# Kernel optimization log

Hardware: AMD Instinct MI355X
Metric: run time of the kernel (lower is better)

The kernel has to match this reference:

```python
import jax, jax.numpy as jnp
import numpy as np

NUM_HEADS = 16
HEAD_DIM = 64
D_MODEL = NUM_HEADS * HEAD_DIM  # 1024
TOP_K_TILES = 8
TILE_SIZE = 16


def setup_inputs() -> dict:
    key = jax.random.key(0)
    kx, kq, kk, kv, ko = jax.random.split(key, 5)
    B, S = 2, 2048
    scale = 1.0 / np.sqrt(D_MODEL)
    return {
        "x": jax.random.normal(kx, (B, S, D_MODEL), dtype=jnp.float32),
        "wq": jax.random.normal(kq, (D_MODEL, NUM_HEADS * HEAD_DIM), dtype=jnp.float32) * scale,
        "wk": jax.random.normal(kk, (D_MODEL, NUM_HEADS * HEAD_DIM), dtype=jnp.float32) * scale,
        "wv": jax.random.normal(kv, (D_MODEL, NUM_HEADS * HEAD_DIM), dtype=jnp.float32) * scale,
        "wo": jax.random.normal(ko, (NUM_HEADS * HEAD_DIM, D_MODEL), dtype=jnp.float32) * scale,
    }


def reference(x, wq, wk, wv, wo):
    B, S, _ = x.shape
    H, D = NUM_HEADS, HEAD_DIM
    q = (x @ wq).reshape(B, S, H, D)
    k = (x @ wk).reshape(B, S, H, D)
    v = (x @ wv).reshape(B, S, H, D)
    logits = jnp.einsum('bqhd,bkhd->bhqk', q, k) / jnp.sqrt(jnp.float32(D))
    causal = jnp.tril(jnp.ones((S, S), dtype=bool))
    logits = jnp.where(causal[None, None, :, :], logits, jnp.float32(-1e10))
    weights = jax.nn.softmax(logits, axis=-1)  # [B,H,S,S]

    # tile pooling + top-k on the last query row (auxiliary output, cached in original)
    last_token_probs = weights[:, :, -1, :]  # [B,H,S]
    pad_len = (TILE_SIZE - S % TILE_SIZE) % TILE_SIZE
    if pad_len > 0:
        last_token_probs = jnp.pad(last_token_probs, ((0, 0), (0, 0), (0, pad_len)))
    num_tiles = last_token_probs.shape[-1] // TILE_SIZE
    tile_scores = last_token_probs.reshape(B, H, num_tiles, TILE_SIZE).max(axis=-1)
    _, top_tile_indices = jax.lax.top_k(tile_scores, TOP_K_TILES)  # side output
    del top_tile_indices  # original stores in a global cache; not returned

    out = jnp.einsum('bhqk,bkhd->bqhd', weights, v).reshape(B, S, H * D)
    return out @ wo
```

## Files before the change

kernel.cpp:

```cpp
#include <hip/hip_runtime.h>
#include <hip/hip_bf16.h>

#define NUM_HEADS 16
#define HEAD_DIM 64
#define DMODEL 1024
#define SEQ 2048
#define BATCH 2
#define MROWS (BATCH*SEQ)

typedef __bf16 bf16;
typedef __bf16 bf16x4 __attribute__((ext_vector_type(4)));
typedef __bf16 bf16x8 __attribute__((ext_vector_type(8)));
typedef float f32x4 __attribute__((ext_vector_type(4)));

#define MFMA16(a, b, c) __builtin_amdgcn_mfma_f32_16x16x32_bf16((a), (b), (c), 0, 0, 0)

#define QSCALE 0.1803368801111444f

__device__ __forceinline__ float fast_exp2(float x) {
    float r;
    asm("v_exp_f32 %0, %1" : "=v"(r) : "v"(x));
    return r;
}

__device__ __forceinline__ void gld16(const void* g, void* l) {
    __builtin_amdgcn_global_load_lds(
        (const __attribute__((address_space(1))) void*)g,
        (__attribute__((address_space(3))) void*)l, 16, 0, 0);
}


__global__ __launch_bounds__(256) void cvt_f32_bf16(const float* __restrict__ in,
                                                    bf16* __restrict__ out, int n4) {
    int i = blockIdx.x * 256 + threadIdx.x;
    if (i >= n4) return;
    float4 v = *(const float4*)(in + (size_t)i * 4);
    bf16x4 o = { (bf16)v.x, (bf16)v.y, (bf16)v.z, (bf16)v.w };
    *(bf16x4*)(out + (size_t)i * 4) = o;
}

__global__ __launch_bounds__(256) void cvt_trans(const float* __restrict__ w0, const float* __restrict__ w1,
                                                 const float* __restrict__ w2, const float* __restrict__ w3,
                                                 bf16* __restrict__ o0, bf16* __restrict__ o1,
                                                 bf16* __restrict__ o2, bf16* __restrict__ o3) {
    const float* w = blockIdx.z == 0 ? w0 : blockIdx.z == 1 ? w1 : blockIdx.z == 2 ? w2 : w3;
    bf16* o = blockIdx.z == 0 ? o0 : blockIdx.z == 1 ? o1 : blockIdx.z == 2 ? o2 : o3;
    __shared__ bf16 tile[64][65];
    int k0 = blockIdx.y * 64, n0 = blockIdx.x * 64;
    int tc = threadIdx.x & 63;
    int tr0 = threadIdx.x >> 6;
#pragma unroll
    for (int i = 0; i < 16; i++) {
        int r = tr0 + i * 4;
        tile[r][tc] = (bf16)w[(size_t)(k0 + r) * DMODEL + n0 + tc];
    }
    __syncthreads();
#pragma unroll
    for (int i = 0; i < 16; i++) {
        int r = tr0 + i * 4;
        o[(size_t)(n0 + r) * DMODEL + k0 + tc] = tile[tc][r];
    }
}


#define BM 128
#define BN 128
#define BK 32

__device__ __forceinline__ void gemm_core(const bf16* __restrict__ A, const bf16* __restrict__ Bt,
                                          int m0, int n0, int Kdim,
                                          bf16* As, bf16* Bs, f32x4 acc[4][4]) {
    int t = threadIdx.x;
    int lane = t & 63;
    int wave = t >> 6;
    int wm = (wave >> 1) * 64;
    int wn = (wave & 1) * 64;
#pragma unroll
    for (int mf = 0; mf < 4; mf++)
#pragma unroll
        for (int nf = 0; nf < 4; nf++) acc[mf][nf] = (f32x4){0.f, 0.f, 0.f, 0.f};

    int arow = lane & 15, kg = lane >> 4;

    for (int k0 = 0; k0 < Kdim; k0 += BK) {
        __syncthreads();
#pragma unroll
        for (int it = 0; it < 2; it++) {
            int chunk = it * 256 + t;
            int rr = chunk >> 2, cc = chunk & 3;
            gld16(A + (size_t)(m0 + rr) * Kdim + k0 + cc * 8, As + chunk * 8);
            gld16(Bt + (size_t)(n0 + rr) * Kdim + k0 + cc * 8, Bs + chunk * 8);
        }
        __syncthreads();
        bf16x8 af[4], bfr[4];
#pragma unroll
        for (int mf = 0; mf < 4; mf++)
            af[mf] = *(const bf16x8*)(As + (wm + mf * 16 + arow) * BK + kg * 8);
#pragma unroll
        for (int nf = 0; nf < 4; nf++)
            bfr[nf] = *(const bf16x8*)(Bs + (wn + nf * 16 + arow) * BK + kg * 8);
#pragma unroll
        for (int mf = 0; mf < 4; mf++)
#pragma unroll
            for (int nf = 0; nf < 4; nf++)
                acc[mf][nf] = MFMA16(af[mf], bfr[nf], acc[mf][nf]);
    }
}

__global__ __launch_bounds__(256) void gemm_qkv(const bf16* __restrict__ xb,
                                                const bf16* __restrict__ wqT, const bf16* __restrict__ wkT,
                                                const bf16* __restrict__ wvT,
                                                bf16* __restrict__ Qh, bf16* __restrict__ Kh,
                                                bf16* __restrict__ Vt) {
    __shared__ __attribute__((aligned(16))) bf16 As[BM * BK];
    __shared__ __attribute__((aligned(16))) bf16 Bs[BN * BK];
    int z = blockIdx.z;
    const bf16* Bt = z == 0 ? wqT : z == 1 ? wkT : wvT;
    int m0 = blockIdx.y * BM, n0 = blockIdx.x * BN;
    f32x4 acc[4][4];
    gemm_core(xb, Bt, m0, n0, DMODEL, As, Bs, acc);

    int lane = threadIdx.x & 63, wave = threadIdx.x >> 6;
    int wm = (wave >> 1) * 64, wn = (wave & 1) * 64;
    int col0 = n0 + wn + (lane & 15);
    int row0 = m0 + wm + (lane >> 4) * 4;
    if (z < 2) {
        bf16* O = z == 0 ? Qh : Kh;
        float scl = z == 0 ? QSCALE : 1.0f;
#pragma unroll
        for (int mf = 0; mf < 4; mf++)
#pragma unroll
            for (int nf = 0; nf < 4; nf++) {
                int n = col0 + nf * 16;
                int mb = row0 + mf * 16;
                int hh = n >> 6, d = n & 63;
#pragma unroll
                for (int i2 = 0; i2 < 4; i2++) {
                    int m = mb + i2;
                    int bb = m >> 11, s = m & 2047;
                    O[(((size_t)bb * NUM_HEADS + hh) * SEQ + s) * HEAD_DIM + d] =
                        (bf16)(acc[mf][nf][i2] * scl);
                }
            }
    } else {
#pragma unroll
        for (int mf = 0; mf < 4; mf++)
#pragma unroll
            for (int nf = 0; nf < 4; nf++) {
                int n = col0 + nf * 16;
                int m = row0 + mf * 16;
                int b = m >> 11, s = m & 2047;
                int h = n >> 6, d = n & 63;
                bf16x4 pack = { (bf16)acc[mf][nf][0], (bf16)acc[mf][nf][1],
                                (bf16)acc[mf][nf][2], (bf16)acc[mf][nf][3] };
                *(bf16x4*)(Vt + ((size_t)(b * NUM_HEADS + h) * HEAD_DIM + d) * SEQ + s) = pack;
            }
    }
}

__global__ __launch_bounds__(256) void gemm_outp(const bf16* __restrict__ at,
                                                 const bf16* __restrict__ woT,
                                                 float* __restrict__ out) {
    __shared__ __attribute__((aligned(16))) bf16 As[BM * BK];
    __shared__ __attribute__((aligned(16))) bf16 Bs[BN * BK];
    int m0 = blockIdx.y * BM, n0 = blockIdx.x * BN;
    f32x4 acc[4][4];
    gemm_core(at, woT, m0, n0, DMODEL, As, Bs, acc);

    int lane = threadIdx.x & 63, wave = threadIdx.x >> 6;
    int wm = (wave >> 1) * 64, wn = (wave & 1) * 64;
    int col0 = n0 + wn + (lane & 15);
    int row0 = m0 + wm + (lane >> 4) * 4;
#pragma unroll
    for (int mf = 0; mf < 4; mf++)
#pragma unroll
        for (int nf = 0; nf < 4; nf++) {
            int n = col0 + nf * 16;
            int mb = row0 + mf * 16;
#pragma unroll
            for (int i2 = 0; i2 < 4; i2++)
                out[(size_t)(mb + i2) * DMODEL + n] = acc[mf][nf][i2];
        }
}

__global__ __launch_bounds__(512, 4) void attn_kernel(const bf16* __restrict__ Qh, const bf16* __restrict__ Kh,
                                                      const bf16* __restrict__ Vt, bf16* __restrict__ attn) {
    __shared__ __attribute__((aligned(16))) bf16 Kl[4 * 64 * 64];
    __shared__ __attribute__((aligned(16))) bf16 Vl[4 * 64 * 64];
    __shared__ __attribute__((aligned(16))) bf16 Pl[8 * 16 * 64];
    int id = blockIdx.x;
    int xcd = id & 7, slot = id >> 3;
    int bh4 = slot >> 4;
    int pairIdx = slot & 15;
    int hb = xcd * 4 + bh4;
    int b = hb >> 4, h = hb & 15;
    int t = threadIdx.x, lane = t & 63, wave = t >> 6;
    int l15 = lane & 15, lg = lane >> 4;
    int strip = wave & 3;
    int gp = wave >> 2;

    const bf16* Qb = Qh + ((size_t)(b * NUM_HEADS + h) * SEQ) * HEAD_DIM;
    const bf16* Kb = Kh + ((size_t)(b * NUM_HEADS + h) * SEQ) * HEAD_DIM;
    const bf16* Vb = Vt + ((size_t)(b * NUM_HEADS + h) * HEAD_DIM) * SEQ;

    char* Pw = (char*)Pl + wave * 2048;
    int swz = (l15 & 7) << 4;
    float* M = (float*)Kl;

    int sc = t;
    int sL = (sc * 16) ^ (((sc >> 3) & 7) << 4);
    int srow = sc >> 3, scole = (sL & 127) >> 1;

    auto STAGE = [&](int kt) {
        int kv0n = kt * 64;
        int bi = kt & 3;
        gld16(Kb + (size_t)(kv0n + srow) * HEAD_DIM + scole, (char*)Kl + bi * 8192 + sc * 16);
        gld16(Vb + (size_t)srow * SEQ + kv0n + scole,        (char*)Vl + bi * 8192 + sc * 16);
    };

#pragma unroll 1
    for (int seg = 0; seg < 2; seg++) {
        int qt = seg ? (31 - pairIdx) : pairIdx;
        int q0w = qt * 64 + strip * 16;
        int nkt = qt + 1;
        int imax = (nkt + 1) >> 1;

        bf16x8 qf[2];
#pragma unroll
        for (int ks = 0; ks < 2; ks++)
            qf[ks] = *(const bf16x8*)(Qb + (size_t)(q0w + l15) * HEAD_DIM + ks * 32 + lg * 8);

        f32x4 oacc[4];
#pragma unroll
        for (int df = 0; df < 4; df++) oacc[df] = (f32x4){0.f, 0.f, 0.f, 0.f};
        float mrun = -1e30f, lrun = 0.f;

        STAGE(0);
        if (nkt > 1) STAGE(1);
        __syncthreads();

#pragma unroll 1
        for (int j = 0; j < imax; j++) {
            int kt = 2 * j + gp;
            int s0 = 2 * j + 2;
            if (s0 < nkt) STAGE(s0);
            if (s0 + 1 < nkt) STAGE(s0 + 1);

            if (kt <= qt) {
                int kv0 = kt * 64;
                const char* KL = (const char*)Kl + (kt & 3) * 8192;
                const char* VL = (const char*)Vl + (kt & 3) * 8192;
                f32x4 st[4];
                __builtin_amdgcn_s_setprio(1);
#pragma unroll
                for (int cf = 0; cf < 4; cf++) {
                    bf16x8 kfr[2];
#pragma unroll
                    for (int ks = 0; ks < 2; ks++) {
                        int off = ((cf * 16 + l15) * 128 + ks * 64 + lg * 16) ^ swz;
                        kfr[ks] = *(const bf16x8*)(KL + off);
                    }
                    st[cf] = (f32x4){0.f, 0.f, 0.f, 0.f};
#pragma unroll
                    for (int ks = 0; ks < 2; ks++)
                        st[cf] = MFMA16(kfr[ks], qf[ks], st[cf]);
                }
                __builtin_amdgcn_s_setprio(0);
                if (kt == qt) {
                    int qrow = q0w + l15;
#pragma unroll
                    for (int cf = 0; cf < 4; cf++)
#pragma unroll
                        for (int i = 0; i < 4; i++) {
                            int kv = kv0 + cf * 16 + lg * 4 + i;
                            if (kv > qrow) st[cf][i] = -1e30f;
                        }
                }
                float m01 = fmaxf(fmaxf(st[0][0], st[0][1]), fmaxf(st[0][2], st[0][3]));
                float m23 = fmaxf(fmaxf(st[1][0], st[1][1]), fmaxf(st[1][2], st[1][3]));
                float m45 = fmaxf(fmaxf(st[2][0], st[2][1]), fmaxf(st[2][2], st[2][3]));
                float m67 = fmaxf(fmaxf(st[3][0], st[3][1]), fmaxf(st[3][2], st[3][3]));
                float mx = fmaxf(fmaxf(m01, m23), fmaxf(m45, m67));
                mx = fmaxf(mx, __shfl_xor(mx, 16, 64));
                mx = fmaxf(mx, __shfl_xor(mx, 32, 64));
                if (!__all(mx <= mrun + 8.0f)) {
                    float mnew = fmaxf(mrun, mx);
                    float alpha = fast_exp2(mrun - mnew);
                    float av[4];
#pragma unroll
                    for (int i = 0; i < 4; i++) av[i] = __shfl(alpha, lg * 4 + i, 64);
#pragma unroll
                    for (int df = 0; df < 4; df++)
#pragma unroll
                        for (int i = 0; i < 4; i++) oacc[df][i] *= av[i];
                    lrun *= alpha;
                    mrun = mnew;
                }
                float psc[4];
                bf16x4 pb[4];
#pragma unroll
                for (int cf = 0; cf < 4; cf++) {
                    float p0 = fast_exp2(st[cf][0] - mrun);
                    float p1 = fast_exp2(st[cf][1] - mrun);
                    float p2 = fast_exp2(st[cf][2] - mrun);
                    float p3 = fast_exp2(st[cf][3] - mrun);
                    psc[cf] = (p0 + p1) + (p2 + p3);
                    pb[cf][0] = (bf16)p0; pb[cf][1] = (bf16)p1;
                    pb[cf][2] = (bf16)p2; pb[cf][3] = (bf16)p3;
                }
                float ps = (psc[0] + psc[1]) + (psc[2] + psc[3]);
                ps += __shfl_xor(ps, 16, 64);
                ps += __shfl_xor(ps, 32, 64);
                lrun += ps;
#pragma unroll
                for (int cf = 0; cf < 4; cf++) {
                    int off = (l15 * 128 + cf * 32 + lg * 8) ^ swz;
                    *(bf16x4*)(Pw + off) = pb[cf];
                }
                bf16x8 pa[2];
#pragma unroll
                for (int ks = 0; ks < 2; ks++) {
                    int off = (l15 * 128 + ks * 64 + lg * 16) ^ swz;
                    pa[ks] = *(const bf16x8*)(Pw + off);
                }
                __builtin_amdgcn_s_setprio(1);
#pragma unroll
                for (int ks = 0; ks < 2; ks++)
#pragma unroll
                    for (int df = 0; df < 4; df++) {
                        int off = ((df * 16 + l15) * 128 + ks * 64 + lg * 16) ^ swz;
                        bf16x8 bv = *(const bf16x8*)(VL + off);
                        oacc[df] = MFMA16(pa[ks], bv, oacc[df]);
                    }
                __builtin_amdgcn_s_setprio(0);
            }
            __syncthreads();
        }

        if (gp == 0) {
#pragma unroll
            for (int df = 0; df < 4; df++)
#pragma unroll
                for (int i = 0; i < 4; i++)
                    M[strip * 1040 + (lg * 4 + i) * 65 + df * 16 + l15] = oacc[df][i];
            if (lg == 0) {
                M[4160 + strip * 16 + l15] = mrun;
                M[4224 + strip * 16 + l15] = lrun;
            }
        }
        __syncthreads();
        if (gp == 1) {
            float mA = M[4160 + strip * 16 + l15];
            float lA = M[4224 + strip * 16 + l15];
            float ms = fmaxf(mrun, mA);
            float aB = fast_exp2(mrun - ms);
            float aA = fast_exp2(mA - ms);
            float lrec = 1.0f / (lrun * aB + lA * aA);
            if (lg == 0) {
                M[4288 + strip * 16 + l15] = aA * lrec;
                M[4352 + strip * 16 + l15] = aB * lrec;
            }
        }
        __syncthreads();
        if (gp == 1) {
#pragma unroll
            for (int df = 0; df < 4; df++)
#pragma unroll
                for (int i = 0; i < 4; i++) {
                    int r = lg * 4 + i;
                    float cA = M[4288 + strip * 16 + r];
                    float cB = M[4352 + strip * 16 + r];
                    float oA = M[strip * 1040 + r * 65 + df * 16 + l15];
                    int qrow = qt * 64 + strip * 16 + r;
                    int d = df * 16 + l15;
                    attn[((size_t)(b * SEQ + qrow)) * DMODEL + h * HEAD_DIM + d] =
                        (bf16)(oacc[df][i] * cB + oA * cA);
                }
        }
        __syncthreads();
    }
}


extern "C" void kernel_launch(void* const* d_in, const int* in_sizes, int n_in,
                              void* d_out, int out_size, void* d_ws, size_t ws_size,
                              hipStream_t stream) {
    const float* x  = (const float*)d_in[0];
    const float* wq = (const float*)d_in[1];
    const float* wk = (const float*)d_in[2];
    const float* wv = (const float*)d_in[3];
    const float* wo = (const float*)d_in[4];
    float* out = (float*)d_out;

    char* w = (char*)d_ws;
    bf16* xb  = (bf16*)(w);
    bf16* wqT = (bf16*)(w + (8ull  << 20));
    bf16* wkT = (bf16*)(w + (10ull << 20));
    bf16* wvT = (bf16*)(w + (12ull << 20));
    bf16* woT = (bf16*)(w + (14ull << 20));
    bf16* Qh  = (bf16*)(w + (16ull << 20));
    bf16* Kh  = (bf16*)(w + (24ull << 20));
    bf16* Vt  = (bf16*)(w + (32ull << 20));
    bf16* at  = (bf16*)(w + (40ull << 20));

    cvt_f32_bf16<<<(MROWS * DMODEL / 4 + 255) / 256, 256, 0, stream>>>(x, xb, MROWS * DMODEL / 4);
    cvt_trans<<<dim3(16, 16, 4), 256, 0, stream>>>(wq, wk, wv, wo, wqT, wkT, wvT, woT);
    gemm_qkv<<<dim3(DMODEL / BN, MROWS / BM, 3), 256, 0, stream>>>(xb, wqT, wkT, wvT, Qh, Kh, Vt);
    attn_kernel<<<dim3(512, 1, 1), 512, 0, stream>>>(Qh, Kh, Vt, at);
    gemm_outp<<<dim3(DMODEL / BN, MROWS / BM), 256, 0, stream>>>(at, woT, out);
}
```

Baseline: 111.2 us.

## Merge conversion kernels, widen GEMM K-tile with swizzled LDS and XCD remap

Fuses the activation cast and the weight transpose-cast into one launch so one kernel launch is saved. The GEMM core doubles BK to 64, halving the number of barrier-separated K iterations, and applies an XOR swizzle to the LDS layout to avoid bank conflicts. It also raises wave priority around the MFMA bursts and remaps block indices so that neighbouring M tiles share an XCD for L2 reuse. The larger LDS tiles raise shared memory per block and may lower occupancy.

```diff
diff --git a/kernel.cpp b/kernel.cpp
--- a/kernel.cpp
+++ b/kernel.cpp
@@ -29,43 +29,46 @@
         (__attribute__((address_space(3))) void*)l, 16, 0, 0);
 }
 
-
-__global__ __launch_bounds__(256) void cvt_f32_bf16(const float* __restrict__ in,
-                                                    bf16* __restrict__ out, int n4) {
-    int i = blockIdx.x * 256 + threadIdx.x;
-    if (i >= n4) return;
-    float4 v = *(const float4*)(in + (size_t)i * 4);
-    bf16x4 o = { (bf16)v.x, (bf16)v.y, (bf16)v.z, (bf16)v.w };
-    *(bf16x4*)(out + (size_t)i * 4) = o;
-}
-
-__global__ __launch_bounds__(256) void cvt_trans(const float* __restrict__ w0, const float* __restrict__ w1,
-                                                 const float* __restrict__ w2, const float* __restrict__ w3,
-                                                 bf16* __restrict__ o0, bf16* __restrict__ o1,
-                                                 bf16* __restrict__ o2, bf16* __restrict__ o3) {
-    const float* w = blockIdx.z == 0 ? w0 : blockIdx.z == 1 ? w1 : blockIdx.z == 2 ? w2 : w3;
-    bf16* o = blockIdx.z == 0 ? o0 : blockIdx.z == 1 ? o1 : blockIdx.z == 2 ? o2 : o3;
+__global__ __launch_bounds__(256) void cvt_all(const float* __restrict__ x,
+                                               const float* __restrict__ w0, const float* __restrict__ w1,
+                                               const float* __restrict__ w2, const float* __restrict__ w3,
+                                               bf16* __restrict__ xb,
+                                               bf16* __restrict__ o0, bf16* __restrict__ o1,
+                                               bf16* __restrict__ o2, bf16* __restrict__ o3) {
     __shared__ bf16 tile[64][65];
-    int k0 = blockIdx.y * 64, n0 = blockIdx.x * 64;
+    int id = blockIdx.x;
+    if (id < 4096) {
+        int i = id * 256 + threadIdx.x;
+        float4 v = *(const float4*)(x + (size_t)i * 4);
+        bf16x4 o = { (bf16)v.x, (bf16)v.y, (bf16)v.z, (bf16)v.w };
+        *(bf16x4*)(xb + (size_t)i * 4) = o;
+        return;
+    }
+    id -= 4096;
+    int z = id >> 8, r = id & 255;
+    int by = r >> 4, bx = r & 15;
+    const float* w = z == 0 ? w0 : z == 1 ? w1 : z == 2 ? w2 : w3;
+    bf16* o = z == 0 ? o0 : z == 1 ? o1 : z == 2 ? o2 : o3;
+    int k0 = by * 64, n0 = bx * 64;
     int tc = threadIdx.x & 63;
     int tr0 = threadIdx.x >> 6;
 #pragma unroll
     for (int i = 0; i < 16; i++) {
-        int r = tr0 + i * 4;
-        tile[r][tc] = (bf16)w[(size_t)(k0 + r) * DMODEL + n0 + tc];
+        int rr = tr0 + i * 4;
+        tile[rr][tc] = (bf16)w[(size_t)(k0 + rr) * DMODEL + n0 + tc];
     }
     __syncthreads();
 #pragma unroll
     for (int i = 0; i < 16; i++) {
-        int r = tr0 + i * 4;
-        o[(size_t)(n0 + r) * DMODEL + k0 + tc] = tile[tc][r];
+        int rr = tr0 + i * 4;
+        o[(size_t)(n0 + rr) * DMODEL + k0 + tc] = tile[tc][rr];
     }
 }
 
 
 #define BM 128
 #define BN 128
-#define BK 32
+#define BK 64
 
 __device__ __forceinline__ void gemm_core(const bf16* __restrict__ A, const bf16* __restrict__ Bt,
                                           int m0, int n0, int Kdim,
@@ -85,26 +88,45 @@
     for (int k0 = 0; k0 < Kdim; k0 += BK) {
         __syncthreads();
 #pragma unroll
-        for (int it = 0; it < 2; it++) {
-            int chunk = it * 256 + t;
-            int rr = chunk >> 2, cc = chunk & 3;
-            gld16(A + (size_t)(m0 + rr) * Kdim + k0 + cc * 8, As + chunk * 8);
-            gld16(Bt + (size_t)(n0 + rr) * Kdim + k0 + cc * 8, Bs + chunk * 8);
-        }
-        __syncthreads();
-        bf16x8 af[4], bfr[4];
-#pragma unroll
-        for (int mf = 0; mf < 4; mf++)
-            af[mf] = *(const bf16x8*)(As + (wm + mf * 16 + arow) * BK + kg * 8);
-#pragma unroll
-        for (int nf = 0; nf < 4; nf++)
-            bfr[nf] = *(const bf16x8*)(Bs + (wn + nf * 16 + arow) * BK + kg * 8);
-#pragma unroll
-        for (int mf = 0; mf < 4; mf++)
-#pragma unroll
-            for (int nf = 0; nf < 4; nf++)
-                acc[mf][nf] = MFMA16(af[mf], bfr[nf], acc[mf][nf]);
-    }
+        for (int it = 0; it < 4; it++) {
+            int c = it * 256 + t;
+            int L = (c * 16) ^ (((c >> 3) & 7) << 4);
+            int rr = c >> 3, ce = (L & 127) >> 1;
+            gld16(A + (size_t)(m0 + rr) * Kdim + k0 + ce, (char*)As + c * 16);
+            gld16(Bt + (size_t)(n0 + rr) * Kdim + k0 + ce, (char*)Bs + c * 16);
+        }
+        __syncthreads();
+#pragma unroll
+        for (int ks = 0; ks < 2; ks++) {
+            bf16x8 af[4], bfr[4];
+#pragma unroll
+            for (int mf = 0; mf < 4; mf++) {
+                int row = wm + mf * 16 + arow;
+                int off = (row * 128 + ks * 64 + kg * 16) ^ ((row & 7) << 4);
+                af[mf] = *(const bf16x8*)((const char*)As + off);
+            }
+#pragma unroll
+            for (int nf = 0; nf < 4; nf++) {
+                int row = wn + nf * 16 + arow;
+                int off = (row * 128 + ks * 64 + kg * 16) ^ ((row & 7) << 4);
+                bfr[nf] = *(const bf16x8*)((const char*)Bs + off);
+            }
+            __builtin_amdgcn_s_setprio(1);
+#pragma unroll
+            for (int mf = 0; mf < 4; mf++)
+#pragma unroll
+                for (int nf = 0; nf < 4; nf++)
+                    acc[mf][nf] = MFMA16(af[mf], bfr[nf], acc[mf][nf]);
+            __builtin_amdgcn_s_setprio(0);
+        }
+    }
+}
+
+__device__ __forceinline__ void xcd_remap(int bx, int by, int& m0, int& n0) {
+    int f = bx + 8 * by;
+    int xcd = f & 7, k = f >> 3;
+    m0 = (xcd * 4 + (k & 3)) * BM;
+    n0 = (k >> 2) * BN;
 }
 
 __global__ __launch_bounds__(256) void gemm_qkv(const bf16* __restrict__ xb,
@@ -116,7 +138,8 @@
     __shared__ __attribute__((aligned(16))) bf16 Bs[BN * BK];
     int z = blockIdx.z;
     const bf16* Bt = z == 0 ? wqT : z == 1 ? wkT : wvT;
-    int m0 = blockIdx.y * BM, n0 = blockIdx.x * BN;
+    int m0, n0;
+    xcd_remap(blockIdx.x, blockIdx.y, m0, n0);
     f32x4 acc[4][4];
     gemm_core(xb, Bt, m0, n0, DMODEL, As, Bs, acc);
 
@@ -163,7 +186,8 @@
                                                  float* __restrict__ out) {
     __shared__ __attribute__((aligned(16))) bf16 As[BM * BK];
     __shared__ __attribute__((aligned(16))) bf16 Bs[BN * BK];
-    int m0 = blockIdx.y * BM, n0 = blockIdx.x * BN;
+    int m0, n0;
+    xcd_remap(blockIdx.x, blockIdx.y, m0, n0);
     f32x4 acc[4][4];
     gemm_core(at, woT, m0, n0, DMODEL, As, Bs, acc);
 
@@ -403,8 +427,7 @@
     bf16* Vt  = (bf16*)(w + (32ull << 20));
     bf16* at  = (bf16*)(w + (40ull << 20));
 
-    cvt_f32_bf16<<<(MROWS * DMODEL / 4 + 255) / 256, 256, 0, stream>>>(x, xb, MROWS * DMODEL / 4);
-    cvt_trans<<<dim3(16, 16, 4), 256, 0, stream>>>(wq, wk, wv, wo, wqT, wkT, wvT, woT);
+    cvt_all<<<5120, 256, 0, stream>>>(x, wq, wk, wv, wo, xb, wqT, wkT, wvT, woT);
     gemm_qkv<<<dim3(DMODEL / BN, MROWS / BM, 3), 256, 0, stream>>>(xb, wqT, wkT, wvT, Qh, Kh, Vt);
     attn_kernel<<<dim3(512, 1, 1), 512, 0, stream>>>(Qh, Kh, Vt, at);
     gemm_outp<<<dim3(DMODEL / BN, MROWS / BM), 256, 0, stream>>>(at, woT, out);
```

New measurement: 114.0 us. 1.03x slower.
